# Performance work log

Hardware: AMD Instinct MI355X
Metric: run time of the kernel (lower is better)

Reference implementation:

```python
import jax, jax.numpy as jnp
import numpy as np

B, N, D_MODEL, H = 2, 512, 256, 8
DH, DS, DE = 8, 8, 8          # hyperbolic / spherical / euclidean component dims
HEAD = D_MODEL // H           # 32
HALF = HEAD // 2              # 16 rope frequencies
KAPPA_S = 1.0                 # spherical curvature
EPS = 1e-6


def setup_inputs() -> dict:
    key = jax.random.key(0)
    ks = jax.random.split(key, 10)
    h = jax.random.normal(ks[0], (B, N, D_MODEL), jnp.float32)
    # manifold coords: hyperbolic part inside Poincare ball, spherical part on unit sphere
    xh = 0.3 * jnp.tanh(jax.random.normal(ks[1], (B, N, DH), jnp.float32))
    xs_raw = jax.random.normal(ks[2], (B, N, DS), jnp.float32)
    xs = xs_raw / jnp.linalg.norm(xs_raw, axis=-1, keepdims=True)
    xe = jax.random.normal(ks[3], (B, N, DE), jnp.float32)
    x = jnp.concatenate([xh, xs, xe], axis=-1)
    def lin(k):
        return 0.05 * jax.random.normal(k, (D_MODEL, D_MODEL), jnp.float32)
    inp = dict(
        h=h, x=x,
        Wq=lin(ks[4]), bq=jnp.zeros((D_MODEL,), jnp.float32),
        Wk=lin(ks[5]), bk=jnp.zeros((D_MODEL,), jnp.float32),
        Wv=lin(ks[6]), bv=jnp.zeros((D_MODEL,), jnp.float32),
        Wo=lin(ks[7]), bo=jnp.zeros((D_MODEL,), jnp.float32),
        w_kernel=jnp.ones((H, 3), jnp.float32),   # torch init: ones(num_heads, num_comp)
        beta=jnp.ones((H,), jnp.float32),
        edge_bias=0.1 * jax.random.normal(ks[8], (B, 1, N, N), jnp.float32),
        node_mask=jnp.ones((B, N), bool),
    )
    return inp


def _pairwise_geometry(x):
    """Returns dh (B,N,N), sdot (B,N,N), de2 (B,N,N), dist (B,N,N)."""
    xh, xs, xe = x[..., :DH], x[..., DH:DH + DS], x[..., DH + DS:]
    # hyperbolic: Poincare-ball distance arccosh(1 + 2|a-b|^2 / ((1-|a|^2)(1-|b|^2)))
    dh2_num = jnp.sum((xh[:, :, None, :] - xh[:, None, :, :]) ** 2, -1)
    one_m = 1.0 - jnp.sum(xh * xh, -1)                               # (B,N)
    arg = 1.0 + 2.0 * dh2_num / (one_m[:, :, None] * one_m[:, None, :])
    dh = jnp.arccosh(jnp.maximum(arg, 1.0 + EPS))
    # spherical: arccos of dot (unit vectors); raw dot kept for the kernel term
    sdot = jnp.einsum('bnd,bmd->bnm', xs, xs)
    ds = jnp.arccos(jnp.clip(sdot, -1.0 + EPS, 1.0 - EPS)) / np.sqrt(KAPPA_S)
    # euclidean: squared distance (kernel uses -d^2; product dist uses d^2)
    de2 = jnp.sum((xe[:, :, None, :] - xe[:, None, :, :]) ** 2, -1)
    dist = jnp.sqrt(dh * dh + ds * ds + de2)
    return dh, sdot, de2, dist


def reference(h, x, Wq, bq, Wk, bk, Wv, bv, Wo, bo, w_kernel, beta, edge_bias, node_mask):
    scale = 1.0 / np.sqrt(HEAD)
    rope_freq = jnp.exp(-np.log(10000.0) * jnp.arange(HALF, dtype=jnp.float32) / HALF)

    def heads(t):  # (B,N,D) -> (B,H,N,head)
        return t.reshape(B, N, H, HEAD).transpose(0, 2, 1, 3)

    Q = heads(h @ Wq.T + bq)
    K = heads(h @ Wk.T + bk)
    V = heads(h @ Wv.T + bv)

    dh, sdot, de2, dist = _pairwise_geometry(x)

    # M-RoPE: rotate Q by pairwise angle theta_ij = omega * d_M(x_i, x_j)
    theta = dist[..., None] * rope_freq                  # (B,N,N,half)
    cos_t = jnp.cos(theta)[:, None]                      # (B,1,N,N,half)
    sin_t = jnp.sin(theta)[:, None]
    q1, q2 = Q[..., 0::2], Q[..., 1::2]                  # (B,H,N,half)
    k1, k2 = K[..., 0::2], K[..., 1::2]
    qk_same = q1[:, :, :, None, :] * k1[:, :, None, :, :] + q2[:, :, :, None, :] * k2[:, :, None, :, :]
    qk_cross = q1[:, :, :, None, :] * k2[:, :, None, :, :] - q2[:, :, :, None, :] * k1[:, :, None, :, :]
    attn = (cos_t * qk_same + sin_t * qk_cross).sum(-1) * scale   # (B,H,N,N)

    # geodesic kernel bias: per-component kernels [H:-d_H, S:k*a.b, E:-|a-b|^2]
    kernel_stack = jnp.stack([-dh, KAPPA_S * sdot, -de2], axis=-1)  # (B,N,N,3)
    geo = jnp.einsum('hc,bnmc->bhnm', w_kernel, kernel_stack)
    attn = attn + beta[None, :, None, None] * geo + edge_bias

    attn = jnp.where(node_mask[:, None, None, :], attn, -jnp.inf)
    p = jax.nn.softmax(attn, axis=-1)
    out = jnp.einsum('bhnm,bhmd->bhnd', p, V).transpose(0, 2, 1, 3).reshape(B, N, D_MODEL)
    return out @ Wo.T + bo
```

## Files before the change

### kernel.cpp

```cpp
#include <hip/hip_runtime.h>

#define N_TOK 512
#define NH 8

typedef __attribute__((ext_vector_type(8))) short short8;
typedef __attribute__((ext_vector_type(4))) short short4v;
typedef __attribute__((ext_vector_type(4))) float f32x4;

__device__ __forceinline__ unsigned short f2bf(float f) {
    union { float f; unsigned u; } v; v.f = f;
    return (unsigned short)((v.u + 0x7FFF + ((v.u >> 16) & 1)) >> 16);
}

__global__ __launch_bounds__(256) void gemm_qkv_mfma(
    const float* __restrict__ A, const float* __restrict__ x,
    const float* __restrict__ Wq, const float* __restrict__ Wk, const float* __restrict__ Wv,
    const float* __restrict__ bq, const float* __restrict__ bk, const float* __restrict__ bv,
    float* __restrict__ Qb, float* __restrict__ KT, float* __restrict__ Vb,
    float* __restrict__ xT)
{
    const int bx = blockIdx.x;
    const int t = threadIdx.x;
    if (bx >= 768) {
        int idx = bx - 768;
        int b = idx / 24, k = idx % 24;
        const float* src = x + (size_t)b * 512 * 24 + k;
        float* dst = xT + (size_t)b * 12288 + k * 512;
        for (int j = t; j < 512; j += 256) dst[j] = src[j * 24];
        return;
    }
    const int z = bx >> 8, rem = bx & 255;
    const int m0 = (rem >> 3) * 32, n0 = (rem & 7) * 32;
    const float* W    = (z == 0) ? Wq : (z == 1) ? Wk : Wv;
    const float* bias = (z == 0) ? bq : (z == 1) ? bk : bv;

    __shared__ short As[32][264];
    __shared__ short Ws[32][264];

    #pragma unroll
    for (int r = 0; r < 8; ++r) {
        int idx = t + 256 * r;
        int row = idx >> 6, c4 = (idx & 63) * 4;
        float4 a = *(const float4*)&A[(m0 + row) * 256 + c4];
        short4v pa = {(short)f2bf(a.x), (short)f2bf(a.y), (short)f2bf(a.z), (short)f2bf(a.w)};
        *(short4v*)&As[row][c4] = pa;
        float4 w = *(const float4*)&W[(n0 + row) * 256 + c4];
        short4v pw = {(short)f2bf(w.x), (short)f2bf(w.y), (short)f2bf(w.z), (short)f2bf(w.w)};
        *(short4v*)&Ws[row][c4] = pw;
    }
    __syncthreads();

    const int w = t >> 6, lane = t & 63;
    const int wm = (w >> 1) * 16, wn = (w & 1) * 16;
    const int frow = lane & 15, kq = lane >> 4;

    f32x4 acc = {0.f, 0.f, 0.f, 0.f};
    #pragma unroll
    for (int k0 = 0; k0 < 8; ++k0) {
        short8 af = *(const short8*)&As[wm + frow][k0 * 32 + kq * 8];
        short8 wf = *(const short8*)&Ws[wn + frow][k0 * 32 + kq * 8];
        if (z == 1) acc = __builtin_amdgcn_mfma_f32_16x16x32_bf16(wf, af, acc, 0, 0, 0);
        else        acc = __builtin_amdgcn_mfma_f32_16x16x32_bf16(af, wf, acc, 0, 0, 0);
    }
    const int col = lane & 15, rq = (lane >> 4) * 4;
    if (z == 1) {
        int tok = m0 + wm + col;
        int bb = tok >> 9, jloc = tok & 511;
        #pragma unroll
        for (int r = 0; r < 4; ++r) {
            int d = n0 + wn + rq + r;
            KT[(size_t)bb * 131072 + d * 512 + jloc] = acc[r] + bias[d];
        }
    } else {
        float* C = (z == 0) ? Qb : Vb;
        float bsv = bias[n0 + wn + col];
        #pragma unroll
        for (int r = 0; r < 4; ++r)
            C[(m0 + wm + rq + r) * 256 + n0 + wn + col] = acc[r] + bsv;
    }
}

__global__ __launch_bounds__(512, 4) void attn_kernel(
    const float* __restrict__ Q, const float* __restrict__ KT, const float* __restrict__ V,
    const float* __restrict__ x, const float* __restrict__ xT,
    const float* __restrict__ wker, const float* __restrict__ beta,
    const float* __restrict__ eb, float* __restrict__ Ao)
{
    const int i0 = blockIdx.x * 2;
    const int b  = blockIdx.y;
    const int t  = threadIdx.x;
    const int lane = t & 63;
    const int h = __builtin_amdgcn_readfirstlane(t >> 6);

    __shared__ float csn[16][2][64][4];
    __shared__ float es[2][NH][128];
    __shared__ float gdh[2][128], gsd[2][128], gde[2][128];

    const float* q0p = Q + (size_t)(b * N_TOK + i0) * 256 + h * 32;
    const float* q1p = q0p + 256;
    const float wk0 = wker[h * 3 + 0], wk1 = wker[h * 3 + 1], wk2 = wker[h * 3 + 2];
    const float bet = beta[h];
    const float scale = 0.17677669529663687f;

    const int gjj = t & 127;
    const int gfh = __builtin_amdgcn_readfirstlane((t >> 7) & 1);
    const int gii = __builtin_amdgcn_readfirstlane(t >> 8);
    const float* xi = x + (size_t)(b * N_TOK + i0 + gii) * 24;
    float onemi = 1.0f;
    #pragma unroll
    for (int k = 0; k < 8; ++k) onemi -= xi[k] * xi[k];
    float frq[8];
    #pragma unroll
    for (int r = 0; r < 8; ++r)
        frq[r] = __expf(-0.5756462732485115f * (float)(gfh * 8 + r));

    float dsum[2] = {0.f, 0.f};
    float accv[2][4] = {{0.f,0.f,0.f,0.f},{0.f,0.f,0.f,0.f}};
    const int jsub = lane >> 3, dq = lane & 7;

    auto geom = [&](int tile) {
        const float* xc = xT + (size_t)b * 12288 + tile * 128 + gjj;
        float xv[24];
        #pragma unroll
        for (int k = 0; k < 24; ++k) xv[k] = xc[k * 512];
        float dh2 = 0.f, oj = 0.f, sd = 0.f, de2 = 0.f;
        #pragma unroll
        for (int k = 0; k < 8; ++k) { float d = xi[k] - xv[k]; dh2 += d * d; oj += xv[k] * xv[k]; }
        #pragma unroll
        for (int k = 0; k < 8; ++k) sd += xi[8 + k] * xv[8 + k];
        #pragma unroll
        for (int k = 0; k < 8; ++k) { float d = xi[16 + k] - xv[16 + k]; de2 += d * d; }
        float arg = 1.0f + 2.0f * dh2 / (onemi * (1.0f - oj));
        arg = fmaxf(arg, 1.0f + 1e-6f);
        float dh = __logf(arg + sqrtf(arg * arg - 1.0f));
        float sdc = fminf(fmaxf(sd, -1.0f + 1e-6f), 1.0f - 1e-6f);
        float dsp = acosf(sdc);
        float dist = sqrtf(dh * dh + dsp * dsp + de2);
        if (gfh == 0) { gdh[gii][gjj] = dh; gsd[gii][gjj] = sd; gde[gii][gjj] = de2; }
        #pragma unroll
        for (int r = 0; r < 8; ++r) {
            float sv, cv;
            __sincosf(dist * frq[r], &sv, &cv);
            *(float2*)&csn[gfh * 8 + r][gii][gjj >> 1][(gjj & 1) * 2] = make_float2(cv, sv);
        }
    };

    geom(0);
    __syncthreads();

    for (int tile = 0; tile < 4; ++tile) {
        {
            float dot[2][2] = {{0.f, 0.f}, {0.f, 0.f}};
            #pragma unroll
            for (int fg = 0; fg < 2; ++fg) {
                const float* kp = KT + (size_t)b * 131072 + (h * 32 + fg * 16) * 512
                                + tile * 128 + 2 * lane;
                float2 kv[16];
                #pragma unroll
                for (int cc = 0; cc < 16; ++cc) kv[cc] = *(const float2*)(kp + cc * 512);
                #pragma unroll
                for (int fl = 0; fl < 8; ++fl) {
                    const int f = fg * 8 + fl;
                    float2 k1 = kv[fl * 2], k2 = kv[fl * 2 + 1];
                    float q10 = q0p[f * 2], q20 = q0p[f * 2 + 1];
                    float q11 = q1p[f * 2], q21 = q1p[f * 2 + 1];
                    float4 c0 = *(const float4*)&csn[f][0][lane][0];
                    float4 c1 = *(const float4*)&csn[f][1][lane][0];
                    dot[0][0] += c0.x * (q10 * k1.x + q20 * k2.x) + c0.y * (q10 * k2.x - q20 * k1.x);
                    dot[0][1] += c0.z * (q10 * k1.y + q20 * k2.y) + c0.w * (q10 * k2.y - q20 * k1.y);
                    dot[1][0] += c1.x * (q11 * k1.x + q21 * k2.x) + c1.y * (q11 * k2.x - q21 * k1.x);
                    dot[1][1] += c1.z * (q11 * k1.y + q21 * k2.y) + c1.w * (q11 * k2.y - q21 * k1.y);
                }
            }
            #pragma unroll
            for (int ii = 0; ii < 2; ++ii) {
                float2 g1 = *(const float2*)&gdh[ii][2 * lane];
                float2 g2 = *(const float2*)&gsd[ii][2 * lane];
                float2 g3 = *(const float2*)&gde[ii][2 * lane];
                float2 e2 = *(const float2*)&eb[((size_t)b * N_TOK + i0 + ii) * N_TOK
                                                + tile * 128 + 2 * lane];
                float s0 = dot[ii][0] * scale + bet * (wk1 * g2.x - wk0 * g1.x - wk2 * g3.x) + e2.x;
                float s1 = dot[ii][1] * scale + bet * (wk1 * g2.y - wk0 * g1.y - wk2 * g3.y) + e2.y;
                float e0 = __expf(s0), e1 = __expf(s1);
                dsum[ii] += e0 + e1;
                *(float2*)&es[ii][h][2 * lane] = make_float2(e0, e1);
            }
        }
        __syncthreads();
        {
            const float* vp = V + (size_t)(b * N_TOK + tile * 128 + jsub) * 256 + h * 32 + dq * 4;
            #pragma unroll
            for (int it = 0; it < 16; ++it) {
                float4 v4 = *(const float4*)(vp + it * 8 * 256);
                int j = it * 8 + jsub;
                float e0 = es[0][h][j], e1 = es[1][h][j];
                accv[0][0] += e0 * v4.x; accv[0][1] += e0 * v4.y;
                accv[0][2] += e0 * v4.z; accv[0][3] += e0 * v4.w;
                accv[1][0] += e1 * v4.x; accv[1][1] += e1 * v4.y;
                accv[1][2] += e1 * v4.z; accv[1][3] += e1 * v4.w;
            }
        }
        if (tile < 3) geom(tile + 1);
        __syncthreads();
    }

    #pragma unroll
    for (int ii = 0; ii < 2; ++ii) {
        float v = dsum[ii];
        v += __shfl_xor(v, 1);  v += __shfl_xor(v, 2);  v += __shfl_xor(v, 4);
        v += __shfl_xor(v, 8);  v += __shfl_xor(v, 16); v += __shfl_xor(v, 32);
        dsum[ii] = 1.0f / v;
    }
    #pragma unroll
    for (int ii = 0; ii < 2; ++ii)
        #pragma unroll
        for (int dd = 0; dd < 4; ++dd) {
            float a = accv[ii][dd];
            a += __shfl_xor(a, 8); a += __shfl_xor(a, 16); a += __shfl_xor(a, 32);
            accv[ii][dd] = a;
        }
    if (jsub == 0) {
        #pragma unroll
        for (int ii = 0; ii < 2; ++ii) {
            float4 o;
            o.x = accv[ii][0] * dsum[ii]; o.y = accv[ii][1] * dsum[ii];
            o.z = accv[ii][2] * dsum[ii]; o.w = accv[ii][3] * dsum[ii];
            *(float4*)&Ao[(size_t)(b * N_TOK + i0 + ii) * 256 + h * 32 + dq * 4] = o;
        }
    }
}

__global__ __launch_bounds__(256) void gemm_out_mfma(
    const float* __restrict__ Ao, const float* __restrict__ Wo,
    const float* __restrict__ bo, float* __restrict__ out)
{
    const int t = threadIdx.x;
    const int m0 = (blockIdx.x >> 3) * 32, n0 = (blockIdx.x & 7) * 32;

    __shared__ short As[32][264];
    __shared__ short Ws[32][264];

    #pragma unroll
    for (int r = 0; r < 8; ++r) {
        int idx = t + 256 * r;
        int row = idx >> 6, c4 = (idx & 63) * 4;
        float4 a = *(const float4*)&Ao[(m0 + row) * 256 + c4];
        short4v pa = {(short)f2bf(a.x), (short)f2bf(a.y), (short)f2bf(a.z), (short)f2bf(a.w)};
        *(short4v*)&As[row][c4] = pa;
        float4 w = *(const float4*)&Wo[(n0 + row) * 256 + c4];
        short4v pw = {(short)f2bf(w.x), (short)f2bf(w.y), (short)f2bf(w.z), (short)f2bf(w.w)};
        *(short4v*)&Ws[row][c4] = pw;
    }
    __syncthreads();

    const int w = t >> 6, lane = t & 63;
    const int wm = (w >> 1) * 16, wn = (w & 1) * 16;
    const int frow = lane & 15, kq = lane >> 4;

    f32x4 acc = {0.f, 0.f, 0.f, 0.f};
    #pragma unroll
    for (int k0 = 0; k0 < 8; ++k0) {
        short8 af = *(const short8*)&As[wm + frow][k0 * 32 + kq * 8];
        short8 wf = *(const short8*)&Ws[wn + frow][k0 * 32 + kq * 8];
        acc = __builtin_amdgcn_mfma_f32_16x16x32_bf16(af, wf, acc, 0, 0, 0);
    }
    const int col = lane & 15, rq = (lane >> 4) * 4;
    float bsv = bo[n0 + wn + col];
    #pragma unroll
    for (int r = 0; r < 4; ++r)
        out[(m0 + wm + rq + r) * 256 + n0 + wn + col] = acc[r] + bsv;
}

extern "C" void kernel_launch(void* const* d_in, const int* in_sizes, int n_in,
                              void* d_out, int out_size, void* d_ws, size_t ws_size,
                              hipStream_t stream) {
    const float* hin  = (const float*)d_in[0];
    const float* x    = (const float*)d_in[1];
    const float* Wq   = (const float*)d_in[2];
    const float* bq   = (const float*)d_in[3];
    const float* Wk   = (const float*)d_in[4];
    const float* bk   = (const float*)d_in[5];
    const float* Wv   = (const float*)d_in[6];
    const float* bv   = (const float*)d_in[7];
    const float* Wo   = (const float*)d_in[8];
    const float* bo   = (const float*)d_in[9];
    const float* wker = (const float*)d_in[10];
    const float* beta = (const float*)d_in[11];
    const float* eb   = (const float*)d_in[12];
    float* out = (float*)d_out;
    float* w   = (float*)d_ws;

    float* Qb = w;
    float* KT = w + 262144;
    float* Vb = w + 524288;
    float* Ao = w + 786432;
    float* xT = w + 1048576;

    hipLaunchKernelGGL(gemm_qkv_mfma, dim3(816), dim3(256), 0, stream,
                       hin, x, Wq, Wk, Wv, bq, bk, bv, Qb, KT, Vb, xT);
    hipLaunchKernelGGL(attn_kernel, dim3(256, 2), dim3(512), 0, stream,
                       Qb, KT, Vb, x, xT, wker, beta, eb, Ao);
    hipLaunchKernelGGL(gemm_out_mfma, dim3(256), dim3(256), 0, stream,
                       Ao, Wo, bo, out);
}
```

Measured before the change: 134.2 us.

## Precompute pairwise geometry once per block and drop redundant per-tile recomputation

Before the tile loop, all 512 threads now compute the hyperbolic, spherical and euclidean geometry and the product distance for both query rows over every key, and store them in shared memory. This removes the old per-tile geometry pass, which both feature-half thread groups ran redundantly. Each tile now only evaluates sincos from the cached distance. acosf is replaced by a polynomial approximation and the divides and square roots by hardware rcp/sqrt intrinsics. One barrier is removed because the exp scores are written and read by the same wave. Shared memory grows by about 16KB, which may reduce how many blocks fit on a CU, and the polynomial slightly changes numerical accuracy.

```diff
diff --git a/kernel.cpp b/kernel.cpp
--- a/kernel.cpp
+++ b/kernel.cpp
@@ -94,21 +94,53 @@
 
     __shared__ float csn[16][2][64][4];
     __shared__ float es[2][NH][128];
-    __shared__ float gdh[2][128], gsd[2][128], gde[2][128];
+    __shared__ float gdh[2][512], gsd[2][512], gde[2][512], gdist[2][512];
+
+    #pragma unroll
+    for (int p = 0; p < 2; ++p) {
+        const int j = t;
+        const float* xi = x + (size_t)(b * N_TOK + i0 + p) * 24;
+        float onemi = 1.0f;
+        #pragma unroll
+        for (int k = 0; k < 8; ++k) onemi -= xi[k] * xi[k];
+        const float* xc = xT + (size_t)b * 12288 + j;
+        float xv[24];
+        #pragma unroll
+        for (int k = 0; k < 24; ++k) xv[k] = xc[k * 512];
+        float dh2 = 0.f, oj = 0.f, sd = 0.f, de2 = 0.f;
+        #pragma unroll
+        for (int k = 0; k < 8; ++k) { float d = xi[k] - xv[k]; dh2 += d * d; oj += xv[k] * xv[k]; }
+        #pragma unroll
+        for (int k = 0; k < 8; ++k) sd += xi[8 + k] * xv[8 + k];
+        #pragma unroll
+        for (int k = 0; k < 8; ++k) { float d = xi[16 + k] - xv[16 + k]; de2 += d * d; }
+        float arg = fmaf(2.0f * dh2, __builtin_amdgcn_rcpf(onemi * (1.0f - oj)), 1.0f);
+        arg = fmaxf(arg, 1.0f + 1e-6f);
+        float dh = __logf(arg + __builtin_amdgcn_sqrtf(fmaf(arg, arg, -1.0f)));
+        float sdc = fminf(fmaxf(sd, -1.0f + 1e-6f), 1.0f - 1e-6f);
+        float ax = fabsf(sdc);
+        float pp = fmaf(ax, -0.0012624911f, 0.0066700901f);
+        pp = fmaf(pp, ax, -0.0170881256f);
+        pp = fmaf(pp, ax,  0.0308918810f);
+        pp = fmaf(pp, ax, -0.0501743046f);
+        pp = fmaf(pp, ax,  0.0889789874f);
+        pp = fmaf(pp, ax, -0.2145988016f);
+        pp = fmaf(pp, ax,  1.5707963050f);
+        pp *= __builtin_amdgcn_sqrtf(1.0f - ax);
+        float dsp = (sdc < 0.f) ? (3.14159265358979f - pp) : pp;
+        float dist = __builtin_amdgcn_sqrtf(fmaf(dh, dh, fmaf(dsp, dsp, de2)));
+        gdh[p][j] = dh; gsd[p][j] = sd; gde[p][j] = de2; gdist[p][j] = dist;
+    }
 
     const float* q0p = Q + (size_t)(b * N_TOK + i0) * 256 + h * 32;
     const float* q1p = q0p + 256;
-    const float wk0 = wker[h * 3 + 0], wk1 = wker[h * 3 + 1], wk2 = wker[h * 3 + 2];
     const float bet = beta[h];
+    const float bw0 = bet * wker[h * 3 + 0], bw1 = bet * wker[h * 3 + 1], bw2 = bet * wker[h * 3 + 2];
     const float scale = 0.17677669529663687f;
 
     const int gjj = t & 127;
     const int gfh = __builtin_amdgcn_readfirstlane((t >> 7) & 1);
     const int gii = __builtin_amdgcn_readfirstlane(t >> 8);
-    const float* xi = x + (size_t)(b * N_TOK + i0 + gii) * 24;
-    float onemi = 1.0f;
-    #pragma unroll
-    for (int k = 0; k < 8; ++k) onemi -= xi[k] * xi[k];
     float frq[8];
     #pragma unroll
     for (int r = 0; r < 8; ++r)
@@ -118,37 +150,19 @@
     float accv[2][4] = {{0.f,0.f,0.f,0.f},{0.f,0.f,0.f,0.f}};
     const int jsub = lane >> 3, dq = lane & 7;
 
-    auto geom = [&](int tile) {
-        const float* xc = xT + (size_t)b * 12288 + tile * 128 + gjj;
-        float xv[24];
-        #pragma unroll
-        for (int k = 0; k < 24; ++k) xv[k] = xc[k * 512];
-        float dh2 = 0.f, oj = 0.f, sd = 0.f, de2 = 0.f;
-        #pragma unroll
-        for (int k = 0; k < 8; ++k) { float d = xi[k] - xv[k]; dh2 += d * d; oj += xv[k] * xv[k]; }
-        #pragma unroll
-        for (int k = 0; k < 8; ++k) sd += xi[8 + k] * xv[8 + k];
-        #pragma unroll
-        for (int k = 0; k < 8; ++k) { float d = xi[16 + k] - xv[16 + k]; de2 += d * d; }
-        float arg = 1.0f + 2.0f * dh2 / (onemi * (1.0f - oj));
-        arg = fmaxf(arg, 1.0f + 1e-6f);
-        float dh = __logf(arg + sqrtf(arg * arg - 1.0f));
-        float sdc = fminf(fmaxf(sd, -1.0f + 1e-6f), 1.0f - 1e-6f);
-        float dsp = acosf(sdc);
-        float dist = sqrtf(dh * dh + dsp * dsp + de2);
-        if (gfh == 0) { gdh[gii][gjj] = dh; gsd[gii][gjj] = sd; gde[gii][gjj] = de2; }
-        #pragma unroll
-        for (int r = 0; r < 8; ++r) {
-            float sv, cv;
-            __sincosf(dist * frq[r], &sv, &cv);
-            *(float2*)&csn[gfh * 8 + r][gii][gjj >> 1][(gjj & 1) * 2] = make_float2(cv, sv);
-        }
-    };
-
-    geom(0);
     __syncthreads();
 
     for (int tile = 0; tile < 4; ++tile) {
+        {
+            float d = gdist[gii][tile * 128 + gjj];
+            #pragma unroll
+            for (int r = 0; r < 8; ++r) {
+                float sv, cv;
+                __sincosf(d * frq[r], &sv, &cv);
+                *(float2*)&csn[gfh * 8 + r][gii][gjj >> 1][(gjj & 1) * 2] = make_float2(cv, sv);
+            }
+        }
+        __syncthreads();
         {
             float dot[2][2] = {{0.f, 0.f}, {0.f, 0.f}};
             #pragma unroll
@@ -174,19 +188,18 @@
             }
             #pragma unroll
             for (int ii = 0; ii < 2; ++ii) {
-                float2 g1 = *(const float2*)&gdh[ii][2 * lane];
-                float2 g2 = *(const float2*)&gsd[ii][2 * lane];
-                float2 g3 = *(const float2*)&gde[ii][2 * lane];
+                float2 g1 = *(const float2*)&gdh[ii][tile * 128 + 2 * lane];
+                float2 g2 = *(const float2*)&gsd[ii][tile * 128 + 2 * lane];
+                float2 g3 = *(const float2*)&gde[ii][tile * 128 + 2 * lane];
                 float2 e2 = *(const float2*)&eb[((size_t)b * N_TOK + i0 + ii) * N_TOK
                                                 + tile * 128 + 2 * lane];
-                float s0 = dot[ii][0] * scale + bet * (wk1 * g2.x - wk0 * g1.x - wk2 * g3.x) + e2.x;
-                float s1 = dot[ii][1] * scale + bet * (wk1 * g2.y - wk0 * g1.y - wk2 * g3.y) + e2.y;
+                float s0 = dot[ii][0] * scale + (bw1 * g2.x - bw0 * g1.x - bw2 * g3.x) + e2.x;
+                float s1 = dot[ii][1] * scale + (bw1 * g2.y - bw0 * g1.y - bw2 * g3.y) + e2.y;
                 float e0 = __expf(s0), e1 = __expf(s1);
                 dsum[ii] += e0 + e1;
                 *(float2*)&es[ii][h][2 * lane] = make_float2(e0, e1);
             }
         }
-        __syncthreads();
         {
             const float* vp = V + (size_t)(b * N_TOK + tile * 128 + jsub) * 256 + h * 32 + dq * 4;
             #pragma unroll
@@ -200,7 +213,6 @@
                 accv[1][2] += e1 * v4.z; accv[1][3] += e1 * v4.w;
             }
         }
-        if (tile < 3) geom(tile + 1);
         __syncthreads();
     }
 
```

Measured after the change: 125.1 us. -6.7%, faster.
